# Kernel optimization log

Hardware: AMD Instinct MI355X
Metric: run time of the kernel (lower is better)

## Reference

```python
import jax, jax.numpy as jnp
import numpy as np

B, T, D = 2, 2048, 1024
H = 16
HD = D // H

def setup_inputs() -> dict:
    key = jax.random.key(0)
    ks = jax.random.split(key, 5)
    s = 1.0 / np.sqrt(D)
    return {
        "x": jax.random.normal(ks[0], (B, T, D), dtype=jnp.float32),
        "Wq": jax.random.normal(ks[1], (D, D), dtype=jnp.float32) * s,
        "bq": jnp.zeros((D,), jnp.float32),
        "Wk": jax.random.normal(ks[2], (D, D), dtype=jnp.float32) * s,
        "bk": jnp.zeros((D,), jnp.float32),
        "Wv": jax.random.normal(ks[3], (D, D), dtype=jnp.float32) * s,
        "bv": jnp.zeros((D,), jnp.float32),
        "Wo": jax.random.normal(ks[4], (D, D), dtype=jnp.float32) * s,
        "bo": jnp.zeros((D,), jnp.float32),
    }

def reference(x, Wq, bq, Wk, bk, Wv, bv, Wo, bo):
    # projections: torch Linear computes x @ W.T + b
    def split_heads(t):  # [B,T,D] -> [B,H,T,HD]
        return t.reshape(B, T, H, HD).transpose(0, 2, 1, 3)
    q = split_heads(x @ Wq.T + bq)
    k = split_heads(x @ Wk.T + bk)
    v = split_heads(x @ Wv.T + bv)
    scale = 1.0 / jnp.sqrt(jnp.asarray(HD, x.dtype))
    scores = jnp.einsum("bhtd,bhsd->bhts", q, k) * scale  # [B,H,T,T]
    causal = jnp.tril(jnp.ones((T, T), bool))
    scores = jnp.where(causal, scores, -jnp.inf)
    attn = jax.nn.softmax(scores, axis=-1)
    out = jnp.einsum("bhts,bhsd->bhtd", attn, v)  # [B,H,T,HD]
    out = out.transpose(0, 2, 1, 3).reshape(B, T, D)
    return out @ Wo.T + bo
```

## Files before the change

### kernel.cpp

```cpp
#include <hip/hip_runtime.h>
#include <hip/hip_bf16.h>

#define B_NUM 2
#define T_LEN 2048
#define D_DIM 1024
#define H_NUM 16
#define HD_DIM 64

#define Q_PRESCALE 0.18033688011112042f

using bf16x8 = __attribute__((ext_vector_type(8))) short;
using f32x4  = __attribute__((ext_vector_type(4))) float;
using u16x4  = __attribute__((ext_vector_type(4))) unsigned short;

__device__ __forceinline__ unsigned short f2bf(float f) {
    union { __hip_bfloat16 b; unsigned short u; } v;
    v.b = __float2bfloat16(f);
    return v.u;
}

__device__ __forceinline__ unsigned pack2bf(float a, float b) {
    union { __hip_bfloat162 h; unsigned u; } v;
    v.h = __float22bfloat162_rn(float2{a, b});
    return v.u;
}

__device__ __forceinline__ void gload16(const unsigned short* g, unsigned short* l) {
    __builtin_amdgcn_global_load_lds(
        (const __attribute__((address_space(1))) void*)g,
        (__attribute__((address_space(3))) void*)l, 16, 0, 0);
}

__global__ __launch_bounds__(256) void cvt5(
    const float* __restrict__ s0, const float* __restrict__ s1, const float* __restrict__ s2,
    const float* __restrict__ s3, const float* __restrict__ s4,
    unsigned short* __restrict__ d0, unsigned short* __restrict__ d1, unsigned short* __restrict__ d2,
    unsigned short* __restrict__ d3, unsigned short* __restrict__ d4,
    int c0, int c1, int c2, int c3, int c4)
{
    const float* src; unsigned short* dst; int cnt;
    switch (blockIdx.z) {
        case 0: src = s0; dst = d0; cnt = c0; break;
        case 1: src = s1; dst = d1; cnt = c1; break;
        case 2: src = s2; dst = d2; cnt = c2; break;
        case 3: src = s3; dst = d3; cnt = c3; break;
        default: src = s4; dst = d4; cnt = c4; break;
    }
    const int stride = gridDim.x * 256 * 4;
    for (int i = (blockIdx.x * 256 + threadIdx.x) * 4; i < cnt; i += stride) {
        float4 v = *(const float4*)(src + i);
        u16x4 o = { f2bf(v.x), f2bf(v.y), f2bf(v.z), f2bf(v.w) };
        *(u16x4*)(dst + i) = o;
    }
}

__device__ __forceinline__ void tile128(
    const unsigned short* __restrict__ A, const unsigned short* __restrict__ Bm,
    int m0, int n0, int K, unsigned short* lds, f32x4 acc[4][4])
{
    const int tid  = threadIdx.x;
    const int lane = tid & 63, w = tid >> 6;
    const int g = lane >> 4, c = lane & 15;
    const int wr = w >> 1, wc = w & 1;
    const int srow = lane >> 2;
    const int sch  = lane & 3;
    const int scsw = sch ^ ((srow >> 1) & 3);
    const int chunk = w * 2;
    const int row0 = chunk * 16 + srow;
    const int row1 = row0 + 16;
    const int rsw = (c >> 1) & 3;

    #pragma unroll
    for (int mi = 0; mi < 4; ++mi)
        #pragma unroll
        for (int ni = 0; ni < 4; ++ni)
            acc[mi][ni] = (f32x4){0.f, 0.f, 0.f, 0.f};

    const unsigned short* gA0 = A  + (size_t)(m0 + row0) * K + scsw * 8;
    const unsigned short* gA1 = A  + (size_t)(m0 + row1) * K + scsw * 8;
    const unsigned short* gB0 = Bm + (size_t)(n0 + row0) * K + scsw * 8;
    const unsigned short* gB1 = Bm + (size_t)(n0 + row1) * K + scsw * 8;

    auto stage = [&](int buf, int k0) {
        unsigned short* bA = lds + buf * 8192;
        unsigned short* bB = bA + 4096;
        gload16(gA0 + k0, bA + chunk * 512);
        gload16(gA1 + k0, bA + (chunk + 1) * 512);
        gload16(gB0 + k0, bB + chunk * 512);
        gload16(gB1 + k0, bB + (chunk + 1) * 512);
    };

    const int nsteps = K / 32;
    stage(0, 0);
    stage(1, 32);
    int buf = 0;
    #pragma unroll 1
    for (int t = 0; t < nsteps; ++t) {
        if (t + 1 < nsteps)
            asm volatile("s_waitcnt vmcnt(4)" ::: "memory");
        else
            asm volatile("s_waitcnt vmcnt(0)" ::: "memory");
        asm volatile("s_waitcnt lgkmcnt(0)" ::: "memory");
        __builtin_amdgcn_s_barrier();
        if (t + 2 < nsteps) {
            int nb = buf + 2; if (nb >= 3) nb -= 3;
            stage(nb, (t + 2) * 32);
        }
        const unsigned short* bA = lds + buf * 8192;
        const unsigned short* bB = bA + 4096;
        bf16x8 af[4], bfr[4];
        #pragma unroll
        for (int mi = 0; mi < 4; ++mi)
            af[mi] = *(const bf16x8*)(bA + (wr * 64 + mi * 16 + c) * 32 + (g ^ rsw) * 8);
        #pragma unroll
        for (int ni = 0; ni < 4; ++ni)
            bfr[ni] = *(const bf16x8*)(bB + (wc * 64 + ni * 16 + c) * 32 + (g ^ rsw) * 8);
        #pragma unroll
        for (int mi = 0; mi < 4; ++mi)
            #pragma unroll
            for (int ni = 0; ni < 4; ++ni)
                acc[mi][ni] = __builtin_amdgcn_mfma_f32_16x16x32_bf16(af[mi], bfr[ni], acc[mi][ni], 0, 0, 0);
        ++buf; if (buf == 3) buf = 0;
    }
}

__global__ __launch_bounds__(256) void gemm_qkv(
    const unsigned short* __restrict__ X,
    const unsigned short* __restrict__ Wq, const unsigned short* __restrict__ Wk,
    const unsigned short* __restrict__ Wv,
    const float* __restrict__ bq, const float* __restrict__ bk, const float* __restrict__ bv,
    unsigned short* __restrict__ Oq, unsigned short* __restrict__ Ok, unsigned short* __restrict__ OvT)
{
    __shared__ __align__(16) unsigned short lds[3 * 8192];
    const int xcd = blockIdx.x & 7;
    const int s   = blockIdx.x >> 3;
    const int mt  = (xcd >> 1) * 8 + s / 12;
    const int rr  = (xcd & 1) * 12 + s % 12;
    const int z   = rr >> 3;
    const int nt  = rr & 7;

    const int lane = threadIdx.x & 63, w = threadIdx.x >> 6;
    const int g = lane >> 4, c = lane & 15;
    const int wr = w >> 1, wc = w & 1;
    f32x4 acc[4][4];

    if (z < 2) {
        const unsigned short* W = z ? Wk : Wq;
        const float* bias       = z ? bk : bq;
        unsigned short* Ob      = z ? Ok : Oq;
        const float oscale      = z ? 1.0f : Q_PRESCALE;
        const int m0 = mt * 128, n0 = nt * 128;
        tile128(X, W, m0, n0, D_DIM, lds, acc);
        #pragma unroll
        for (int mi = 0; mi < 4; ++mi) {
            #pragma unroll
            for (int ni = 0; ni < 4; ++ni) {
                const int col = n0 + wc * 64 + ni * 16 + c;
                const int h = col >> 6, hd = col & 63;
                const float bb = bias[col];
                #pragma unroll
                for (int r = 0; r < 4; ++r) {
                    const int row = m0 + wr * 64 + mi * 16 + g * 4 + r;
                    const int b_ = row >> 11, t = row & (T_LEN - 1);
                    Ob[((size_t)((b_ * H_NUM + h) * T_LEN + t)) * HD_DIM + hd] =
                        f2bf((acc[mi][ni][r] + bb) * oscale);
                }
            }
        }
    } else {
        const int m0 = nt * 128, n0 = mt * 128;
        tile128(Wv, X, m0, n0, D_DIM, lds, acc);
        #pragma unroll
        for (int mi = 0; mi < 4; ++mi) {
            #pragma unroll
            for (int ni = 0; ni < 4; ++ni) {
                const int j = n0 + wc * 64 + ni * 16 + c;
                const int b_ = j >> 11, t = j & (T_LEN - 1);
                #pragma unroll
                for (int r = 0; r < 4; ++r) {
                    const int f = m0 + wr * 64 + mi * 16 + g * 4 + r;
                    OvT[(size_t)(b_ * D_DIM + f) * T_LEN + t] = f2bf(acc[mi][ni][r] + bv[f]);
                }
            }
        }
    }
}

__global__ __launch_bounds__(256) void gemm_out(
    const unsigned short* __restrict__ A, const unsigned short* __restrict__ W,
    const float* __restrict__ bias, float* __restrict__ Out)
{
    __shared__ __align__(16) unsigned short lds[3 * 8192];
    const int bsw = (blockIdx.x & 7) * 32 + (blockIdx.x >> 3);
    const int mt = bsw >> 3, nt = bsw & 7;
    const int lane = threadIdx.x & 63, w = threadIdx.x >> 6;
    const int g = lane >> 4, c = lane & 15;
    const int m0 = mt * 128, n0 = nt * 128;
    f32x4 acc[4][4];
    tile128(A, W, m0, n0, D_DIM, lds, acc);
    const int wr = w >> 1, wc = w & 1;
    #pragma unroll
    for (int mi = 0; mi < 4; ++mi) {
        #pragma unroll
        for (int ni = 0; ni < 4; ++ni) {
            const int col = n0 + wc * 64 + ni * 16 + c;
            const float bb = bias[col];
            #pragma unroll
            for (int r = 0; r < 4; ++r) {
                const int row = m0 + wr * 64 + mi * 16 + g * 4 + r;
                Out[(size_t)row * D_DIM + col] = acc[mi][ni][r] + bb;
            }
        }
    }
}

__global__ __launch_bounds__(256, 4) void attn(
    const unsigned short* __restrict__ Q, const unsigned short* __restrict__ K,
    const unsigned short* __restrict__ VT, unsigned short* __restrict__ O)
{
    __shared__ __align__(16) unsigned short kv_lds[2][2][64 * 64];
    __shared__ __align__(16) unsigned short plbuf[4][16 * 64];
    const int tid = threadIdx.x, lane = tid & 63, w = tid >> 6;
    const int g = lane >> 4, c = lane & 15;

    const int gid = blockIdx.x;
    const int bh = gid & 31;
    const int jt = (gid < 512) ? (31 - (gid >> 5)) : ((gid - 512) >> 5);
    const int q0b = jt * 64;
    const int qw0 = q0b + w * 16;

    const unsigned short* Qb = Q  + (size_t)bh * T_LEN * HD_DIM;
    const unsigned short* Kb = K  + (size_t)bh * T_LEN * HD_DIM;
    const unsigned short* Vb = VT + (size_t)bh * HD_DIM * T_LEN;
    unsigned short* pl = plbuf[w];

    bf16x8 qf[2];
    #pragma unroll
    for (int kk = 0; kk < 2; ++kk)
        qf[kk] = *(const bf16x8*)(Qb + (size_t)(qw0 + c) * HD_DIM + kk * 32 + g * 8);

    f32x4 acc[4];
    #pragma unroll
    for (int ni = 0; ni < 4; ++ni) acc[ni] = (f32x4){0.f, 0.f, 0.f, 0.f};
    float m2 = -1e30f, l2 = 0.f;

    auto stage = [&](int buf, int kv0) {
        unsigned short* kb = &kv_lds[buf][0][0];
        unsigned short* vb = &kv_lds[buf][1][0];
        #pragma unroll
        for (int rnd = 0; rnd < 2; ++rnd) {
            const int bch = rnd * 256 + w * 64;
            const int row = (bch >> 3) + (lane >> 3);
            const int sc16 = (lane & 7) ^ (row & 7);
            gload16(Kb + (size_t)(kv0 + row) * HD_DIM + sc16 * 8, kb + bch * 8);
            gload16(Vb + (size_t)row * T_LEN + kv0 + sc16 * 8,   vb + bch * 8);
        }
    };

    const int ntiles = jt + 1;
    stage(0, 0);
    if (ntiles > 1) stage(1, 64);
    int cur = 0;
    #pragma unroll 1
    for (int t = 0; t < ntiles; ++t) {
        const int kv0 = t << 6;
        if (t + 1 < ntiles)
            asm volatile("s_waitcnt vmcnt(4)" ::: "memory");
        else
            asm volatile("s_waitcnt vmcnt(0)" ::: "memory");
        __builtin_amdgcn_s_barrier();
        const unsigned short* kb = &kv_lds[cur][0][0];
        const unsigned short* vb = &kv_lds[cur][1][0];

        f32x4 sf[4];
        #pragma unroll
        for (int st = 0; st < 4; ++st) {
            const int rr = st * 16 + c;
            bf16x8 kf0 = *(const bf16x8*)(kb + rr * 64 + ((g       ^ (c & 7)) * 8));
            bf16x8 kf1 = *(const bf16x8*)(kb + rr * 64 + (((4 + g) ^ (c & 7)) * 8));
            f32x4 s = (f32x4){0.f, 0.f, 0.f, 0.f};
            s = __builtin_amdgcn_mfma_f32_16x16x32_bf16(kf0, qf[0], s, 0, 0, 0);
            s = __builtin_amdgcn_mfma_f32_16x16x32_bf16(kf1, qf[1], s, 0, 0, 0);
            sf[st] = s;
        }
        if (t == jt) {
            const int qg = qw0 + c;
            #pragma unroll
            for (int st = 0; st < 4; ++st)
                #pragma unroll
                for (int r = 0; r < 4; ++r) {
                    const int kvg = kv0 + st * 16 + g * 4 + r;
                    sf[st][r] = (kvg <= qg) ? sf[st][r] : -1e30f;
                }
        }
        float ma = fmaxf(fmaxf(sf[0][0], sf[0][1]), sf[0][2]);
        float mb = fmaxf(fmaxf(sf[0][3], sf[1][0]), sf[1][1]);
        float mc = fmaxf(fmaxf(sf[1][2], sf[1][3]), sf[2][0]);
        float md = fmaxf(fmaxf(sf[2][1], sf[2][2]), sf[2][3]);
        float me = fmaxf(fmaxf(sf[3][0], sf[3][1]), sf[3][2]);
        float mx = fmaxf(fmaxf(fmaxf(ma, mb), fmaxf(mc, md)), fmaxf(me, sf[3][3]));
        mx = fmaxf(mx, __shfl_xor(mx, 16));
        mx = fmaxf(mx, __shfl_xor(mx, 32));
        if (__any(mx > m2 + 8.f)) {
            const float mnew = fmaxf(m2, mx);
            const float alpha = __builtin_amdgcn_exp2f(m2 - mnew);
            float ar[4];
            #pragma unroll
            for (int r = 0; r < 4; ++r) ar[r] = __shfl(alpha, g * 4 + r);
            l2 *= alpha;
            #pragma unroll
            for (int ni = 0; ni < 4; ++ni)
                #pragma unroll
                for (int r = 0; r < 4; ++r) acc[ni][r] *= ar[r];
            m2 = mnew;
        }
        float sum = 0.f;
        #pragma unroll
        for (int st = 0; st < 4; ++st)
            #pragma unroll
            for (int r = 0; r < 4; ++r) {
                const float p = __builtin_amdgcn_exp2f(sf[st][r] - m2);
                sf[st][r] = p;
                sum += p;
            }
        sum += __shfl_xor(sum, 16);
        sum += __shfl_xor(sum, 32);
        l2 += sum;
        #pragma unroll
        for (int st = 0; st < 4; ++st) {
            uint2 pk;
            pk.x = pack2bf(sf[st][0], sf[st][1]);
            pk.y = pack2bf(sf[st][2], sf[st][3]);
            const int idx = (c * 64 + st * 16 + g * 4) ^ ((c & 7) << 3);
            *(uint2*)(pl + idx) = pk;
        }
        asm volatile("" ::: "memory");
        bf16x8 pa[2];
        #pragma unroll
        for (int kk = 0; kk < 2; ++kk) {
            const int ridx = (c * 64 + kk * 32 + g * 8) ^ ((c & 7) << 3);
            pa[kk] = *(const bf16x8*)(pl + ridx);
        }
        #pragma unroll
        for (int ni = 0; ni < 4; ++ni) {
            const int rr = ni * 16 + c;
            bf16x8 vf0 = *(const bf16x8*)(vb + rr * 64 + ((g       ^ (c & 7)) * 8));
            bf16x8 vf1 = *(const bf16x8*)(vb + rr * 64 + (((4 + g) ^ (c & 7)) * 8));
            acc[ni] = __builtin_amdgcn_mfma_f32_16x16x32_bf16(pa[0], vf0, acc[ni], 0, 0, 0);
            acc[ni] = __builtin_amdgcn_mfma_f32_16x16x32_bf16(pa[1], vf1, acc[ni], 0, 0, 0);
        }
        asm volatile("s_waitcnt lgkmcnt(0)" ::: "memory");
        __builtin_amdgcn_s_barrier();
        if (t + 2 < ntiles) stage(cur, (t + 2) << 6);
        cur ^= 1;
    }

    const float linv = 1.0f / l2;
    float lr[4];
    #pragma unroll
    for (int r = 0; r < 4; ++r) lr[r] = __shfl(linv, g * 4 + r);
    const int b_ = bh >> 4, h = bh & 15;
    #pragma unroll
    for (int ni = 0; ni < 4; ++ni)
        #pragma unroll
        for (int r = 0; r < 4; ++r) {
            const int q = qw0 + g * 4 + r;
            O[(size_t)(b_ * T_LEN + q) * D_DIM + h * HD_DIM + ni * 16 + c] =
                f2bf(acc[ni][r] * lr[r]);
        }
}

extern "C" void kernel_launch(void* const* d_in, const int* in_sizes, int n_in,
                              void* d_out, int out_size, void* d_ws, size_t ws_size,
                              hipStream_t stream)
{
    const float* x  = (const float*)d_in[0];
    const float* Wq = (const float*)d_in[1];
    const float* bq = (const float*)d_in[2];
    const float* Wk = (const float*)d_in[3];
    const float* bk = (const float*)d_in[4];
    const float* Wv = (const float*)d_in[5];
    const float* bv = (const float*)d_in[6];
    const float* Wo = (const float*)d_in[7];
    const float* bo = (const float*)d_in[8];
    float* out = (float*)d_out;

    char* ws = (char*)d_ws;
    const size_t MB = 1u << 20;
    unsigned short* xb  = (unsigned short*)(ws + 0 * MB);
    unsigned short* wqb = (unsigned short*)(ws + 8 * MB);
    unsigned short* wkb = (unsigned short*)(ws + 10 * MB);
    unsigned short* wvb = (unsigned short*)(ws + 12 * MB);
    unsigned short* wob = (unsigned short*)(ws + 14 * MB);
    unsigned short* qw  = (unsigned short*)(ws + 16 * MB);
    unsigned short* kw  = (unsigned short*)(ws + 24 * MB);
    unsigned short* vtw = (unsigned short*)(ws + 32 * MB);
    unsigned short* ow  = (unsigned short*)(ws + 40 * MB);

    cvt5<<<dim3(1024, 1, 5), dim3(256), 0, stream>>>(
        x, Wq, Wk, Wv, Wo, xb, wqb, wkb, wvb, wob,
        B_NUM * T_LEN * D_DIM, D_DIM * D_DIM, D_DIM * D_DIM, D_DIM * D_DIM, D_DIM * D_DIM);

    gemm_qkv<<<dim3(768), dim3(256), 0, stream>>>(
        xb, wqb, wkb, wvb, bq, bk, bv, qw, kw, vtw);

    attn<<<dim3(1024), dim3(256), 0, stream>>>(qw, kw, vtw, ow);

    gemm_out<<<dim3(256), dim3(256), 0, stream>>>(
        ow, wob, bo, out);
}
```

Baseline: 98.50 us.

## Use 256x128 tiles with 512-thread blocks for QKV projection GEMM

The QKV projection GEMM moves from 128x128 tiles with 256 threads to 256x128 tiles with 512 threads (8 waves), halving the block count to 384. Each K-step stages two A rows per wave and one B row into a larger triple-buffered LDS region, so the B tile is shared across twice as many output rows. The aim is less global/LDS traffic per FLOP. In exchange LDS use per block grows and there are fewer blocks to balance across CUs, and the block-to-tile remapping changes the XCD locality pattern.

Measured after the change: 98.37 us. Within noise of the previous version (-0.1%).

```diff
diff --git a/kernel.cpp b/kernel.cpp
--- a/kernel.cpp
+++ b/kernel.cpp
@@ -124,33 +124,96 @@
     }
 }
 
-__global__ __launch_bounds__(256) void gemm_qkv(
+__device__ __forceinline__ void tile256x128(
+    const unsigned short* __restrict__ A, const unsigned short* __restrict__ Bm,
+    int m0, int n0, int K, unsigned short* lds, f32x4 acc[4][4])
+{
+    const int tid  = threadIdx.x;
+    const int lane = tid & 63, w = tid >> 6;
+    const int g = lane >> 4, c = lane & 15;
+    const int wr = w >> 1, wc = w & 1;
+    const int srow = lane >> 2;
+    const int sch  = lane & 3;
+    const int scsw = sch ^ ((srow >> 1) & 3);
+    const int rsw = (c >> 1) & 3;
+
+    #pragma unroll
+    for (int mi = 0; mi < 4; ++mi)
+        #pragma unroll
+        for (int ni = 0; ni < 4; ++ni)
+            acc[mi][ni] = (f32x4){0.f, 0.f, 0.f, 0.f};
+
+    const unsigned short* gA0 = A  + (size_t)(m0 + w * 32 + srow) * K + scsw * 8;
+    const unsigned short* gA1 = A  + (size_t)(m0 + w * 32 + 16 + srow) * K + scsw * 8;
+    const unsigned short* gB0 = Bm + (size_t)(n0 + w * 16 + srow) * K + scsw * 8;
+
+    auto stage = [&](int buf, int k0) {
+        unsigned short* bA = lds + buf * 12288;
+        unsigned short* bB = bA + 8192;
+        gload16(gA0 + k0, bA + (w * 2) * 512);
+        gload16(gA1 + k0, bA + (w * 2 + 1) * 512);
+        gload16(gB0 + k0, bB + w * 512);
+    };
+
+    const int nsteps = K / 32;
+    stage(0, 0);
+    stage(1, 32);
+    int buf = 0;
+    #pragma unroll 1
+    for (int t = 0; t < nsteps; ++t) {
+        if (t + 1 < nsteps)
+            asm volatile("s_waitcnt vmcnt(3)" ::: "memory");
+        else
+            asm volatile("s_waitcnt vmcnt(0)" ::: "memory");
+        asm volatile("s_waitcnt lgkmcnt(0)" ::: "memory");
+        __builtin_amdgcn_s_barrier();
+        if (t + 2 < nsteps) {
+            int nb = buf + 2; if (nb >= 3) nb -= 3;
+            stage(nb, (t + 2) * 32);
+        }
+        const unsigned short* bA = lds + buf * 12288;
+        const unsigned short* bB = bA + 8192;
+        bf16x8 af[4], bfr[4];
+        #pragma unroll
+        for (int mi = 0; mi < 4; ++mi)
+            af[mi] = *(const bf16x8*)(bA + (wr * 64 + mi * 16 + c) * 32 + (g ^ rsw) * 8);
+        #pragma unroll
+        for (int ni = 0; ni < 4; ++ni)
+            bfr[ni] = *(const bf16x8*)(bB + (wc * 64 + ni * 16 + c) * 32 + (g ^ rsw) * 8);
+        #pragma unroll
+        for (int mi = 0; mi < 4; ++mi)
+            #pragma unroll
+            for (int ni = 0; ni < 4; ++ni)
+                acc[mi][ni] = __builtin_amdgcn_mfma_f32_16x16x32_bf16(af[mi], bfr[ni], acc[mi][ni], 0, 0, 0);
+        ++buf; if (buf == 3) buf = 0;
+    }
+}
+
+__global__ __launch_bounds__(512, 4) void gemm_qkv(
     const unsigned short* __restrict__ X,
     const unsigned short* __restrict__ Wq, const unsigned short* __restrict__ Wk,
     const unsigned short* __restrict__ Wv,
     const float* __restrict__ bq, const float* __restrict__ bk, const float* __restrict__ bv,
     unsigned short* __restrict__ Oq, unsigned short* __restrict__ Ok, unsigned short* __restrict__ OvT)
 {
-    __shared__ __align__(16) unsigned short lds[3 * 8192];
-    const int xcd = blockIdx.x & 7;
-    const int s   = blockIdx.x >> 3;
-    const int mt  = (xcd >> 1) * 8 + s / 12;
-    const int rr  = (xcd & 1) * 12 + s % 12;
-    const int z   = rr >> 3;
-    const int nt  = rr & 7;
+    __shared__ __align__(16) unsigned short lds[3 * 12288];
+    const int bsw = (blockIdx.x & 7) * 48 + (blockIdx.x >> 3);
 
     const int lane = threadIdx.x & 63, w = threadIdx.x >> 6;
     const int g = lane >> 4, c = lane & 15;
     const int wr = w >> 1, wc = w & 1;
     f32x4 acc[4][4];
 
-    if (z < 2) {
+    if (bsw < 256) {
+        const int z  = bsw >> 7;
+        const int r  = bsw & 127;
+        const int mt = r >> 3, nt = r & 7;
         const unsigned short* W = z ? Wk : Wq;
         const float* bias       = z ? bk : bq;
         unsigned short* Ob      = z ? Ok : Oq;
         const float oscale      = z ? 1.0f : Q_PRESCALE;
-        const int m0 = mt * 128, n0 = nt * 128;
-        tile128(X, W, m0, n0, D_DIM, lds, acc);
+        const int m0 = mt * 256, n0 = nt * 128;
+        tile256x128(X, W, m0, n0, D_DIM, lds, acc);
         #pragma unroll
         for (int mi = 0; mi < 4; ++mi) {
             #pragma unroll
@@ -159,17 +222,19 @@
                 const int h = col >> 6, hd = col & 63;
                 const float bb = bias[col];
                 #pragma unroll
-                for (int r = 0; r < 4; ++r) {
-                    const int row = m0 + wr * 64 + mi * 16 + g * 4 + r;
+                for (int r2 = 0; r2 < 4; ++r2) {
+                    const int row = m0 + wr * 64 + mi * 16 + g * 4 + r2;
                     const int b_ = row >> 11, t = row & (T_LEN - 1);
                     Ob[((size_t)((b_ * H_NUM + h) * T_LEN + t)) * HD_DIM + hd] =
-                        f2bf((acc[mi][ni][r] + bb) * oscale);
+                        f2bf((acc[mi][ni][r2] + bb) * oscale);
                 }
             }
         }
     } else {
-        const int m0 = nt * 128, n0 = mt * 128;
-        tile128(Wv, X, m0, n0, D_DIM, lds, acc);
+        const int r  = bsw - 256;
+        const int mt = r >> 5, nt = r & 31;
+        const int m0 = mt * 256, n0 = nt * 128;
+        tile256x128(Wv, X, m0, n0, D_DIM, lds, acc);
         #pragma unroll
         for (int mi = 0; mi < 4; ++mi) {
             #pragma unroll
@@ -177,9 +242,9 @@
                 const int j = n0 + wc * 64 + ni * 16 + c;
                 const int b_ = j >> 11, t = j & (T_LEN - 1);
                 #pragma unroll
-                for (int r = 0; r < 4; ++r) {
-                    const int f = m0 + wr * 64 + mi * 16 + g * 4 + r;
-                    OvT[(size_t)(b_ * D_DIM + f) * T_LEN + t] = f2bf(acc[mi][ni][r] + bv[f]);
+                for (int r2 = 0; r2 < 4; ++r2) {
+                    const int f = m0 + wr * 64 + mi * 16 + g * 4 + r2;
+                    OvT[(size_t)(b_ * D_DIM + f) * T_LEN + t] = f2bf(acc[mi][ni][r2] + bv[f]);
                 }
             }
         }
@@ -401,7 +466,7 @@
         x, Wq, Wk, Wv, Wo, xb, wqb, wkb, wvb, wob,
         B_NUM * T_LEN * D_DIM, D_DIM * D_DIM, D_DIM * D_DIM, D_DIM * D_DIM, D_DIM * D_DIM);
 
-    gemm_qkv<<<dim3(768), dim3(256), 0, stream>>>(
+    gemm_qkv<<<dim3(384), dim3(512), 0, stream>>>(
         xb, wqb, wkb, wvb, bq, bk, bv, qw, kw, vtw);
 
     attn<<<dim3(1024), dim3(256), 0, stream>>>(qw, kw, vtw, ow);
```

## Fuse Q and K projections into one block sharing the X tile

Applied to the files above, without the earlier changes.

Q and K projection tiles are now computed by a single block that loads each X tile once and runs MFMAs against both Wq and Wk, keeping two accumulator sets. The grid shrinks from 768 to 512 blocks: 256 blocks do fused Q/K and 256 do V. This removes redundant X loads from global memory into LDS. In exchange it doubles accumulator register pressure in the fused blocks and enlarges LDS to 72KB, which can lower occupancy. It also makes the work uneven, since fused blocks do twice the MFMA work of V blocks.

Measured after the change: 100.7 us. 2.3% more time.

```diff
diff --git a/kernel.cpp b/kernel.cpp
--- a/kernel.cpp
+++ b/kernel.cpp
@@ -56,7 +56,7 @@
 
 __device__ __forceinline__ void tile128(
     const unsigned short* __restrict__ A, const unsigned short* __restrict__ Bm,
-    int m0, int n0, int K, unsigned short* lds, f32x4 acc[4][4])
+    int m0, int n0, int K, unsigned short* lds, int ldsstride, f32x4 acc[4][4])
 {
     const int tid  = threadIdx.x;
     const int lane = tid & 63, w = tid >> 6;
@@ -82,7 +82,7 @@
     const unsigned short* gB1 = Bm + (size_t)(n0 + row1) * K + scsw * 8;
 
     auto stage = [&](int buf, int k0) {
-        unsigned short* bA = lds + buf * 8192;
+        unsigned short* bA = lds + buf * ldsstride;
         unsigned short* bB = bA + 4096;
         gload16(gA0 + k0, bA + chunk * 512);
         gload16(gA1 + k0, bA + (chunk + 1) * 512);
@@ -106,7 +106,7 @@
             int nb = buf + 2; if (nb >= 3) nb -= 3;
             stage(nb, (t + 2) * 32);
         }
-        const unsigned short* bA = lds + buf * 8192;
+        const unsigned short* bA = lds + buf * ldsstride;
         const unsigned short* bB = bA + 4096;
         bf16x8 af[4], bfr[4];
         #pragma unroll
@@ -131,45 +131,117 @@
     const float* __restrict__ bq, const float* __restrict__ bk, const float* __restrict__ bv,
     unsigned short* __restrict__ Oq, unsigned short* __restrict__ Ok, unsigned short* __restrict__ OvT)
 {
-    __shared__ __align__(16) unsigned short lds[3 * 8192];
+    __shared__ __align__(16) unsigned short lds[3 * 12288];
     const int xcd = blockIdx.x & 7;
     const int s   = blockIdx.x >> 3;
-    const int mt  = (xcd >> 1) * 8 + s / 12;
-    const int rr  = (xcd & 1) * 12 + s % 12;
-    const int z   = rr >> 3;
-    const int nt  = rr & 7;
-
-    const int lane = threadIdx.x & 63, w = threadIdx.x >> 6;
+
+    const int tid  = threadIdx.x;
+    const int lane = tid & 63, w = tid >> 6;
     const int g = lane >> 4, c = lane & 15;
     const int wr = w >> 1, wc = w & 1;
-    f32x4 acc[4][4];
-
-    if (z < 2) {
-        const unsigned short* W = z ? Wk : Wq;
-        const float* bias       = z ? bk : bq;
-        unsigned short* Ob      = z ? Ok : Oq;
-        const float oscale      = z ? 1.0f : Q_PRESCALE;
+
+    if (s < 32) {
+        const int idx = xcd * 32 + s;
+        const int mt = idx >> 3, nt = idx & 7;
         const int m0 = mt * 128, n0 = nt * 128;
-        tile128(X, W, m0, n0, D_DIM, lds, acc);
+
+        const int srow = lane >> 2;
+        const int sch  = lane & 3;
+        const int scsw = sch ^ ((srow >> 1) & 3);
+        const int chunk = w * 2;
+        const int row0 = chunk * 16 + srow;
+        const int row1 = row0 + 16;
+        const int rsw = (c >> 1) & 3;
+
+        f32x4 accq[4][4], acck[4][4];
+        #pragma unroll
+        for (int mi = 0; mi < 4; ++mi)
+            #pragma unroll
+            for (int ni = 0; ni < 4; ++ni) {
+                accq[mi][ni] = (f32x4){0.f, 0.f, 0.f, 0.f};
+                acck[mi][ni] = (f32x4){0.f, 0.f, 0.f, 0.f};
+            }
+
+        const unsigned short* gA0 = X  + (size_t)(m0 + row0) * D_DIM + scsw * 8;
+        const unsigned short* gA1 = X  + (size_t)(m0 + row1) * D_DIM + scsw * 8;
+        const unsigned short* gQ0 = Wq + (size_t)(n0 + row0) * D_DIM + scsw * 8;
+        const unsigned short* gQ1 = Wq + (size_t)(n0 + row1) * D_DIM + scsw * 8;
+        const unsigned short* gK0 = Wk + (size_t)(n0 + row0) * D_DIM + scsw * 8;
+        const unsigned short* gK1 = Wk + (size_t)(n0 + row1) * D_DIM + scsw * 8;
+
+        auto stage = [&](int buf, int k0) {
+            unsigned short* bA = lds + buf * 12288;
+            unsigned short* bQ = bA + 4096;
+            unsigned short* bK = bA + 8192;
+            gload16(gA0 + k0, bA + chunk * 512);
+            gload16(gA1 + k0, bA + (chunk + 1) * 512);
+            gload16(gQ0 + k0, bQ + chunk * 512);
+            gload16(gQ1 + k0, bQ + (chunk + 1) * 512);
+            gload16(gK0 + k0, bK + chunk * 512);
+            gload16(gK1 + k0, bK + (chunk + 1) * 512);
+        };
+
+        const int nsteps = D_DIM / 32;
+        stage(0, 0);
+        stage(1, 32);
+        int buf = 0;
+        #pragma unroll 1
+        for (int t = 0; t < nsteps; ++t) {
+            if (t + 1 < nsteps)
+                asm volatile("s_waitcnt vmcnt(6)" ::: "memory");
+            else
+                asm volatile("s_waitcnt vmcnt(0)" ::: "memory");
+            asm volatile("s_waitcnt lgkmcnt(0)" ::: "memory");
+            __builtin_amdgcn_s_barrier();
+            if (t + 2 < nsteps) {
+                int nb = buf + 2; if (nb >= 3) nb -= 3;
+                stage(nb, (t + 2) * 32);
+            }
+            const unsigned short* bA = lds + buf * 12288;
+            const unsigned short* bQ = bA + 4096;
+            const unsigned short* bK = bA + 8192;
+            bf16x8 af[4], bqf[4], bkf[4];
+            #pragma unroll
+            for (int mi = 0; mi < 4; ++mi)
+                af[mi] = *(const bf16x8*)(bA + (wr * 64 + mi * 16 + c) * 32 + (g ^ rsw) * 8);
+            #pragma unroll
+            for (int ni = 0; ni < 4; ++ni) {
+                bqf[ni] = *(const bf16x8*)(bQ + (wc * 64 + ni * 16 + c) * 32 + (g ^ rsw) * 8);
+                bkf[ni] = *(const bf16x8*)(bK + (wc * 64 + ni * 16 + c) * 32 + (g ^ rsw) * 8);
+            }
+            #pragma unroll
+            for (int mi = 0; mi < 4; ++mi)
+                #pragma unroll
+                for (int ni = 0; ni < 4; ++ni) {
+                    accq[mi][ni] = __builtin_amdgcn_mfma_f32_16x16x32_bf16(af[mi], bqf[ni], accq[mi][ni], 0, 0, 0);
+                    acck[mi][ni] = __builtin_amdgcn_mfma_f32_16x16x32_bf16(af[mi], bkf[ni], acck[mi][ni], 0, 0, 0);
+                }
+            ++buf; if (buf == 3) buf = 0;
+        }
+
         #pragma unroll
         for (int mi = 0; mi < 4; ++mi) {
             #pragma unroll
             for (int ni = 0; ni < 4; ++ni) {
                 const int col = n0 + wc * 64 + ni * 16 + c;
                 const int h = col >> 6, hd = col & 63;
-                const float bb = bias[col];
+                const float bbq = bq[col], bbk = bk[col];
                 #pragma unroll
                 for (int r = 0; r < 4; ++r) {
                     const int row = m0 + wr * 64 + mi * 16 + g * 4 + r;
                     const int b_ = row >> 11, t = row & (T_LEN - 1);
-                    Ob[((size_t)((b_ * H_NUM + h) * T_LEN + t)) * HD_DIM + hd] =
-                        f2bf((acc[mi][ni][r] + bb) * oscale);
+                    const size_t base = ((size_t)((b_ * H_NUM + h) * T_LEN + t)) * HD_DIM + hd;
+                    Oq[base] = f2bf((accq[mi][ni][r] + bbq) * Q_PRESCALE);
+                    Ok[base] = f2bf(acck[mi][ni][r] + bbk);
                 }
             }
         }
     } else {
-        const int m0 = nt * 128, n0 = mt * 128;
-        tile128(Wv, X, m0, n0, D_DIM, lds, acc);
+        const int idx = xcd * 32 + (s - 32);
+        const int mt = idx >> 5, nt = idx & 31;
+        const int m0 = mt * 128, n0 = nt * 128;
+        f32x4 acc[4][4];
+        tile128(Wv, X, m0, n0, D_DIM, lds, 12288, acc);
         #pragma unroll
         for (int mi = 0; mi < 4; ++mi) {
             #pragma unroll
@@ -197,7 +269,7 @@
     const int g = lane >> 4, c = lane & 15;
     const int m0 = mt * 128, n0 = nt * 128;
     f32x4 acc[4][4];
-    tile128(A, W, m0, n0, D_DIM, lds, acc);
+    tile128(A, W, m0, n0, D_DIM, lds, 8192, acc);
     const int wr = w >> 1, wc = w & 1;
     #pragma unroll
     for (int mi = 0; mi < 4; ++mi) {
@@ -401,7 +473,7 @@
         x, Wq, Wk, Wv, Wo, xb, wqb, wkb, wvb, wob,
         B_NUM * T_LEN * D_DIM, D_DIM * D_DIM, D_DIM * D_DIM, D_DIM * D_DIM, D_DIM * D_DIM);
 
-    gemm_qkv<<<dim3(768), dim3(256), 0, stream>>>(
+    gemm_qkv<<<dim3(512), dim3(256), 0, stream>>>(
         xb, wqb, wkb, wvb, bq, bk, bv, qw, kw, vtw);
 
     attn<<<dim3(1024), dim3(256), 0, stream>>>(qw, kw, vtw, ow);
```
